# Optimization experiments

Hardware: AMD Instinct MI355X
Metric: run time of the kernel (lower is better)

Reference implementation:

```python
import jax, jax.numpy as jnp
import numpy as np

NUM_HEADS = 12


def _rel_pos_table(q_size, k_size, rel_pos):
    # rel_pos: (2*q_size-1, head_dim); q_size == k_size here so no interpolation.
    q_coords = jnp.arange(q_size)[:, None] * max(k_size / q_size, 1.0)
    k_coords = jnp.arange(k_size)[None, :] * max(q_size / k_size, 1.0)
    rel = (q_coords - k_coords + (k_size - 1) * max(q_size / k_size, 1.0)).astype(jnp.int32)
    return rel_pos[rel]  # (q_size, k_size, head_dim)


def setup_inputs() -> dict:
    key = jax.random.key(0)
    ks = jax.random.split(key, 7)
    B, H, W, D = 1, 64, 64, 768
    hd = D // NUM_HEADS
    x = jax.random.normal(ks[0], (B, H, W, D), dtype=jnp.float32)
    w_qkv = jax.random.normal(ks[1], (3 * D, D), dtype=jnp.float32) * (1.0 / np.sqrt(D))
    b_qkv = jnp.zeros((3 * D,), dtype=jnp.float32)
    w_proj = jax.random.normal(ks[2], (D, D), dtype=jnp.float32) * (1.0 / np.sqrt(D))
    b_proj = jnp.zeros((D,), dtype=jnp.float32)
    rel_pos_h = jax.random.normal(ks[3], (2 * H - 1, hd), dtype=jnp.float32) * 0.02
    rel_pos_w = jax.random.normal(ks[4], (2 * W - 1, hd), dtype=jnp.float32) * 0.02
    return {"x": x, "w_qkv": w_qkv, "b_qkv": b_qkv, "w_proj": w_proj,
            "b_proj": b_proj, "rel_pos_h": rel_pos_h, "rel_pos_w": rel_pos_w}


def reference(x, w_qkv, b_qkv, w_proj, b_proj, rel_pos_h, rel_pos_w):
    b, h, w, d = x.shape
    nh = NUM_HEADS
    hd = d // nh
    scale = hd ** -0.5
    # combined qkv projection: (b,h,w,3d) -> (3, b*nh, h*w, hd)
    qkv = x @ w_qkv.T + b_qkv
    qkv = qkv.reshape(b, h * w, 3, nh, hd).transpose(2, 0, 3, 1, 4)
    qkv = qkv.reshape(3, b * nh, h * w, hd)
    q, k, v = qkv[0], qkv[1], qkv[2]
    attn = (q * scale) @ k.swapaxes(-2, -1)  # (b*nh, hw, hw)
    # decomposed 2D relative position bias
    rh = _rel_pos_table(h, h, rel_pos_h)  # (h, h, hd)
    rw = _rel_pos_table(w, w, rel_pos_w)  # (w, w, hd)
    r_q = q.reshape(b * nh, h, w, hd)
    rel_h = jnp.einsum('bhwc,hkc->bhwk', r_q, rh)
    rel_w = jnp.einsum('bhwc,wkc->bhwk', r_q, rw)
    attn = (attn.reshape(b * nh, h, w, h, w)
            + rel_h[:, :, :, :, None]
            + rel_w[:, :, :, None, :]).reshape(b * nh, h * w, h * w)
    attn = jax.nn.softmax(attn, axis=-1)
    out = attn @ v  # (b*nh, hw, hd)
    out = out.reshape(b, nh, h, w, hd).transpose(0, 2, 3, 1, 4).reshape(b, h, w, d)
    return out @ w_proj.T + b_proj
```

## Files before the change

### kernel.cpp

```cpp
#include <hip/hip_runtime.h>
#include <hip/hip_bf16.h>
#include <stdint.h>


typedef unsigned short u16;
typedef unsigned int   u32;
typedef __attribute__((ext_vector_type(8))) short s8v;
typedef __attribute__((ext_vector_type(4))) float f4v;
typedef __attribute__((ext_vector_type(4))) unsigned short us4;
typedef __attribute__((ext_vector_type(8))) unsigned short us8;
typedef __attribute__((ext_vector_type(2))) unsigned int u32x2;

#define DEVI static __device__ __forceinline__

constexpr int   NTOK   = 4096;
constexpr int   DM     = 768;
constexpr float LOG2E_F = 1.4426950408889634f;
constexpr float KSCALE  = 0.18033688011112042f;

#if __has_builtin(__builtin_amdgcn_exp2f)
#define EXP2(x) __builtin_amdgcn_exp2f(x)
#else
#define EXP2(x) exp2f(x)
#endif

DEVI u16 f2bf(float x){
  u32 u = __builtin_bit_cast(u32, x);
  u32 r = (u + 0x7FFFu + ((u >> 16) & 1u)) >> 16;
  return (u16)r;
}
DEVI float bf2f(u16 h){
  u32 u = ((u32)h) << 16;
  return __builtin_bit_cast(float, u);
}
DEVI u32 cvtpk(float lo, float hi){
  u32 r;
  asm("v_cvt_pk_bf16_f32 %0, %1, %2" : "=v"(r) : "v"(lo), "v"(hi));
  return r;
}

typedef const __attribute__((address_space(1))) u32* gp1;
typedef __attribute__((address_space(3))) u32* lp3;
DEVI void gload_lds16(const void* g, void* l){
  __builtin_amdgcn_global_load_lds((gp1)g, (lp3)l, 16, 0, 0);
}

DEVI f4v MFMA16(s8v a, s8v b, f4v c){
  return __builtin_amdgcn_mfma_f32_16x16x32_bf16(a, b, c, 0, 0, 0);
}

__global__ void k_split(const float* __restrict__ in, u16* __restrict__ hi,
                        u16* __restrict__ lo, int n4){
  int i = blockIdx.x * blockDim.x + threadIdx.x;
  int stride = gridDim.x * blockDim.x;
  for (; i < n4; i += stride){
    f4v v = ((const f4v*)in)[i];
    us4 h, l;
#pragma unroll
    for (int j = 0; j < 4; ++j){
      u16 hb = f2bf(v[j]);
      h[j] = hb;
      l[j] = f2bf(v[j] - bf2f(hb));
    }
    ((us4*)hi)[i] = h;
    ((us4*)lo)[i] = l;
  }
}

template<int EPI>
__global__ __launch_bounds__(256)
void k_gemm(const u16* __restrict__ Ah, const u16* __restrict__ Al,
            const u16* __restrict__ Bh, const u16* __restrict__ Bl,
            const float* __restrict__ bias, int K,
            u16* __restrict__ Qh, u16* __restrict__ Ql,
            u16* __restrict__ Kh, u16* __restrict__ Kl,
            float* __restrict__ Vf, float* __restrict__ Cout)
{
  __shared__ __align__(16) unsigned char sm[32768];
  const int t = threadIdx.x;
  const int lane = t & 63, wid = t >> 6;
  const int l15 = lane & 15, g = lane >> 4;
  const int wr = wid >> 1, wc = wid & 1;
  const int m0 = blockIdx.y * 128, n0 = blockIdx.x * 128;

  const char* aGh[2]; const char* aGl[2]; const char* bGh[2]; const char* bGl[2];
#pragma unroll
  for (int ch = 0; ch < 2; ++ch){
    int p = ch * 4096 + t * 16;
    int pair = p >> 7, w = p & 127;
    int u = w ^ ((pair & 7) << 4);
    int row = 2 * pair + (u >> 6);
    int cb  = u & 63;
    aGh[ch] = (const char*)Ah + (size_t)(m0 + row) * K * 2 + cb;
    aGl[ch] = (const char*)Al + (size_t)(m0 + row) * K * 2 + cb;
    bGh[ch] = (const char*)Bh + (size_t)(n0 + row) * K * 2 + cb;
    bGl[ch] = (const char*)Bl + (size_t)(n0 + row) * K * 2 + cb;
  }
  const int axor = ((l15 & 1) * 64 + g * 16) ^ (((l15 >> 1) & 7) << 4);
  const int abase = (wr * 32 + (l15 >> 1)) * 128 + axor;
  const int bbase = 16384 + (wc * 32 + (l15 >> 1)) * 128 + axor;

  f4v acc[4][4] = {};
  const int KSTEPS = K >> 5;
  for (int kt = 0; kt < KSTEPS; ++kt){
    __syncthreads();
#pragma unroll
    for (int ch = 0; ch < 2; ++ch){
      gload_lds16(aGh[ch], sm + 0     + ch*4096 + wid*1024);
      gload_lds16(aGl[ch], sm + 8192  + ch*4096 + wid*1024);
      gload_lds16(bGh[ch], sm + 16384 + ch*4096 + wid*1024);
      gload_lds16(bGl[ch], sm + 24576 + ch*4096 + wid*1024);
      aGh[ch] += 64; aGl[ch] += 64; bGh[ch] += 64; bGl[ch] += 64;
    }
    __syncthreads();
    s8v af[4][2];
#pragma unroll
    for (int mi = 0; mi < 4; ++mi){
      af[mi][0] = *(const s8v*)(sm + abase + mi*1024);
      af[mi][1] = *(const s8v*)(sm + abase + mi*1024 + 8192);
    }
#pragma unroll
    for (int ni = 0; ni < 4; ++ni){
      s8v bh = *(const s8v*)(sm + bbase + ni*1024);
      s8v bl = *(const s8v*)(sm + bbase + ni*1024 + 8192);
#pragma unroll
      for (int mi = 0; mi < 4; ++mi){
        acc[mi][ni] = MFMA16(af[mi][0], bh, acc[mi][ni]);
        acc[mi][ni] = MFMA16(af[mi][0], bl, acc[mi][ni]);
        acc[mi][ni] = MFMA16(af[mi][1], bh, acc[mi][ni]);
      }
    }
  }

  if (EPI == 2){
#pragma unroll
    for (int ni = 0; ni < 4; ++ni){
      int col = n0 + wc*64 + ni*16 + l15;
      float bq = bias[col];
#pragma unroll
      for (int mi = 0; mi < 4; ++mi){
        int rw0 = m0 + wr*64 + mi*16 + g*4;
#pragma unroll
        for (int r = 0; r < 4; ++r)
          Cout[(size_t)(rw0 + r) * DM + col] = acc[mi][ni][r] + bq;
      }
    }
  } else {
#pragma unroll
    for (int ni = 0; ni < 4; ++ni){
      int colb = n0 + wc*64 + ni*16;
      float bq = bias[colb + l15];
      int which = colb / DM;
      int rem   = colb % DM;
      int head  = rem >> 6;
      int c     = (rem & 63) + l15;
#pragma unroll
      for (int mi = 0; mi < 4; ++mi){
        int n = m0 + wr*64 + mi*16 + g*4;
#pragma unroll
        for (int r = 0; r < 4; ++r){
          float v = acc[mi][ni][r] + bq;
          size_t idx = ((size_t)head * NTOK + (n + r)) * 64 + c;
          if (which == 0){
            u16 hb = f2bf(v);
            Qh[idx] = hb; Ql[idx] = f2bf(v - bf2f(hb));
          } else if (which == 1){
            float v2 = v * KSCALE;
            u16 hb = f2bf(v2);
            Kh[idx] = hb; Kl[idx] = f2bf(v2 - bf2f(hb));
          } else {
            Vf[idx] = v;
          }
        }
      }
    }
  }
}

__global__ void k_vtrans(const float* __restrict__ Vf, u16* __restrict__ Vth){
  __shared__ float tile[64][65];
  int h = blockIdx.y, nt = blockIdx.x;
  int t = threadIdx.x;
  {
    int r = t >> 2, c0 = (t & 3) * 16;
    const float* src = Vf + ((size_t)h * NTOK + nt*64 + r) * 64 + c0;
#pragma unroll
    for (int j = 0; j < 4; ++j){
      f4v v = *(const f4v*)(src + j*4);
      tile[r][c0+j*4+0] = v[0]; tile[r][c0+j*4+1] = v[1];
      tile[r][c0+j*4+2] = v[2]; tile[r][c0+j*4+3] = v[3];
    }
  }
  __syncthreads();
  {
    int c = t >> 2, b = (t & 3) * 16;
    us8 o0, o1;
#pragma unroll
    for (int i = 0; i < 16; ++i){
      u16 bv = f2bf(tile[b + i][c]);
      if (i < 8) o0[i] = bv; else o1[i-8] = bv;
    }
    u16* dst = Vth + ((size_t)h * 64 + c) * NTOK + nt*64 + b;
    *(us8*)(dst)     = o0;
    *(us8*)(dst + 8) = o1;
  }
}

__global__ void k_relh(const u16* __restrict__ Qh, const u16* __restrict__ Ql,
                       const float* __restrict__ rp, float* __restrict__ R){
  __shared__ float qs[64][68];
  __shared__ float rs[64][68];
  int h = blockIdx.y, qh = blockIdx.x;
  int t = threadIdx.x;
  {
    int r = t >> 2, c0 = (t & 3) * 16;
    size_t qb = ((size_t)h * NTOK + qh*64 + r) * 64 + c0;
#pragma unroll
    for (int j = 0; j < 2; ++j){
      us8 vh = *(const us8*)(Qh + qb + j*8);
      us8 vl = *(const us8*)(Ql + qb + j*8);
#pragma unroll
      for (int e = 0; e < 8; ++e)
        qs[r][c0 + j*8 + e] = bf2f(vh[e]) + bf2f(vl[e]);
    }
    const float* pr = rp + (size_t)(qh - r + 63) * 64 + c0;
#pragma unroll
    for (int j = 0; j < 4; ++j){
      f4v v = *(const f4v*)(pr + j*4);
      rs[r][c0+j*4+0]=v[0]; rs[r][c0+j*4+1]=v[1];
      rs[r][c0+j*4+2]=v[2]; rs[r][c0+j*4+3]=v[3];
    }
  }
  __syncthreads();
  int qw = t >> 2, k0 = t & 3;
  float acc[16] = {};
  for (int c = 0; c < 64; c += 4){
    f4v qv = *(const f4v*)(&qs[qw][c]);
#pragma unroll
    for (int i = 0; i < 16; ++i){
      f4v rv = *(const f4v*)(&rs[k0 + 4*i][c]);
      acc[i] += qv[0]*rv[0] + qv[1]*rv[1] + qv[2]*rv[2] + qv[3]*rv[3];
    }
  }
  float* o = R + ((size_t)h * NTOK + qh*64 + qw) * 64;
#pragma unroll
  for (int i = 0; i < 16; ++i) o[k0 + 4*i] = acc[i] * LOG2E_F;
}

__global__ void k_relw(const u16* __restrict__ Qh, const u16* __restrict__ Ql,
                       const float* __restrict__ rp, float* __restrict__ R){
  __shared__ float qs[64][68];
  __shared__ float rs[64][68];
  int h = blockIdx.y, qw = blockIdx.x;
  int t = threadIdx.x;
  {
    int r = t >> 2, c0 = (t & 3) * 16;
    size_t qb = ((size_t)h * NTOK + r*64 + qw) * 64 + c0;
#pragma unroll
    for (int j = 0; j < 2; ++j){
      us8 vh = *(const us8*)(Qh + qb + j*8);
      us8 vl = *(const us8*)(Ql + qb + j*8);
#pragma unroll
      for (int e = 0; e < 8; ++e)
        qs[r][c0 + j*8 + e] = bf2f(vh[e]) + bf2f(vl[e]);
    }
    const float* pr = rp + (size_t)(qw - r + 63) * 64 + c0;
#pragma unroll
    for (int j = 0; j < 4; ++j){
      f4v v = *(const f4v*)(pr + j*4);
      rs[r][c0+j*4+0]=v[0]; rs[r][c0+j*4+1]=v[1];
      rs[r][c0+j*4+2]=v[2]; rs[r][c0+j*4+3]=v[3];
    }
  }
  __syncthreads();
  int qh = t >> 2, k0 = t & 3;
  float acc[16] = {};
  for (int c = 0; c < 64; c += 4){
    f4v qv = *(const f4v*)(&qs[qh][c]);
#pragma unroll
    for (int i = 0; i < 16; ++i){
      f4v rv = *(const f4v*)(&rs[k0 + 4*i][c]);
      acc[i] += qv[0]*rv[0] + qv[1]*rv[1] + qv[2]*rv[2] + qv[3]*rv[3];
    }
  }
  float* o = R + ((size_t)h * NTOK + qh*64 + qw) * 64;
#pragma unroll
  for (int i = 0; i < 16; ++i) o[k0 + 4*i] = acc[i] * LOG2E_F;
}

__global__ __launch_bounds__(256)
void k_attn(const u16* __restrict__ Qh, const u16* __restrict__ Ql,
            const u16* __restrict__ Kh, const u16* __restrict__ Kl,
            const u16* __restrict__ Vth,
            const float* __restrict__ Rh, const float* __restrict__ Rw,
            u16* __restrict__ Oh, u16* __restrict__ Ol)
{
  __shared__ __align__(16) unsigned char sm[33792];
  const int t = threadIdx.x;
  const int lane = t & 63, wid = t >> 6;
  const int l15 = lane & 15, g = lane >> 4;
  const int h = blockIdx.y;
  const int qrow0 = blockIdx.x * 64 + wid * 16;

  const char* kGh[2]; const char* kGl[2]; const char* vG[2];
#pragma unroll
  for (int ch = 0; ch < 2; ++ch){
    int p = ch * 4096 + t * 16;
    int row = p >> 7;
    int cb  = (p & 127) ^ ((row & 7) << 4);
    kGh[ch] = (const char*)Kh + ((size_t)h * NTOK + row) * 128 + cb;
    kGl[ch] = (const char*)Kl + ((size_t)h * NTOK + row) * 128 + cb;
    vG[ch]  = (const char*)Vth + ((size_t)h * 64 + row) * (NTOK*2) + cb;
  }

  const size_t qoff = ((size_t)h * NTOK + qrow0 + l15) * 64 + g * 8;
  s8v qh0 = *(const s8v*)(Qh + qoff);
  s8v qh1 = *(const s8v*)(Qh + qoff + 32);
  s8v ql0 = *(const s8v*)(Ql + qoff);
  s8v ql1 = *(const s8v*)(Ql + qoff + 32);

  const int xr  = (l15 & 7) << 4;
  const int kb0 = l15 * 128 + ((g * 16)      ^ xr);
  const int kb1 = l15 * 128 + ((g * 16 + 64) ^ xr);
  const int vb0 = 16384 + kb0;
  const int vb1 = 16384 + kb1;
  const int pbase = 24576 + wid * 2304 + l15 * 144;

  const float* rwp = Rw + ((size_t)h * NTOK + qrow0 + l15) * 64 + 4*g;
  f4v rwv[4];
#pragma unroll
  for (int tt = 0; tt < 4; ++tt) rwv[tt] = *(const f4v*)(rwp + 16*tt);
  const float* rhp = Rh + ((size_t)h * NTOK + qrow0 + l15) * 64;

  f4v o[4] = {};
  float m2 = -1.0e30f, ls = 0.f;

  for (int it = 0; it < 64; ++it){
    __syncthreads();
#pragma unroll
    for (int ch = 0; ch < 2; ++ch){
      gload_lds16(kGh[ch], sm + 0     + ch*4096 + wid*1024);
      gload_lds16(kGl[ch], sm + 8192  + ch*4096 + wid*1024);
      gload_lds16(vG[ch],  sm + 16384 + ch*4096 + wid*1024);
      kGh[ch] += 8192; kGl[ch] += 8192; vG[ch] += 128;
    }
    __syncthreads();

    const float rhv = rhp[it];

    f4v s[4];
#pragma unroll
    for (int tt = 0; tt < 4; ++tt){
      s8v kh_0 = *(const s8v*)(sm + kb0 + tt*2048);
      s8v kh_1 = *(const s8v*)(sm + kb1 + tt*2048);
      s8v kl_0 = *(const s8v*)(sm + kb0 + tt*2048 + 8192);
      s8v kl_1 = *(const s8v*)(sm + kb1 + tt*2048 + 8192);
      f4v a = {};
      a = MFMA16(kh_0, qh0, a);
      a = MFMA16(kh_1, qh1, a);
      a = MFMA16(kl_0, qh0, a);
      a = MFMA16(kl_1, qh1, a);
      a = MFMA16(kh_0, ql0, a);
      a = MFMA16(kh_1, ql1, a);
      s[tt] = a;
    }
    float pm = -1.0e30f;
#pragma unroll
    for (int tt = 0; tt < 4; ++tt){
#pragma unroll
      for (int r = 0; r < 4; ++r){
        s[tt][r] += rhv + rwv[tt][r];
        pm = fmaxf(pm, s[tt][r]);
      }
    }
    pm = fmaxf(pm, __shfl_xor(pm, 16, 64));
    pm = fmaxf(pm, __shfl_xor(pm, 32, 64));
    const float mn = fmaxf(m2, pm);
    const float fr = EXP2(m2 - mn);
    m2 = mn;
    float ps = 0.f;
#pragma unroll
    for (int tt = 0; tt < 4; ++tt){
#pragma unroll
      for (int r = 0; r < 4; ++r){
        float p = EXP2(s[tt][r] - m2);
        s[tt][r] = p;
        ps += p;
      }
    }
    ps += __shfl_xor(ps, 16, 64);
    ps += __shfl_xor(ps, 32, 64);
    ls = ls * fr + ps;

#pragma unroll
    for (int tt = 0; tt < 4; ++tt){
      u32x2 w2;
      w2[0] = cvtpk(s[tt][0], s[tt][1]);
      w2[1] = cvtpk(s[tt][2], s[tt][3]);
      *(u32x2*)(sm + pbase + 8*g + 32*tt) = w2;
    }
#pragma unroll
    for (int dt = 0; dt < 4; ++dt){
#pragma unroll
      for (int r = 0; r < 4; ++r) o[dt][r] *= fr;
    }
    s8v pa0 = *(const s8v*)(sm + pbase + 16*g);
    s8v pa1 = *(const s8v*)(sm + pbase + 16*g + 64);
#pragma unroll
    for (int dt = 0; dt < 4; ++dt){
      s8v v0 = *(const s8v*)(sm + vb0 + dt*2048);
      s8v v1 = *(const s8v*)(sm + vb1 + dt*2048);
      o[dt] = MFMA16(v0, pa0, o[dt]);
      o[dt] = MFMA16(v1, pa1, o[dt]);
    }
  }

  const float inv = 1.0f / ls;
  const size_t obase = (size_t)(qrow0 + l15) * DM + h*64 + 4*g;
#pragma unroll
  for (int dt = 0; dt < 4; ++dt){
    us4 hv, lv;
#pragma unroll
    for (int r = 0; r < 4; ++r){
      float v = o[dt][r] * inv;
      u16 hb = f2bf(v);
      hv[r] = hb;
      lv[r] = f2bf(v - bf2f(hb));
    }
    *(us4*)(Oh + obase + 16*dt) = hv;
    *(us4*)(Ol + obase + 16*dt) = lv;
  }
}

extern "C" void kernel_launch(void* const* d_in, const int* in_sizes, int n_in,
                              void* d_out, int out_size, void* d_ws, size_t ws_size,
                              hipStream_t stream){
  (void)in_sizes; (void)n_in; (void)out_size; (void)ws_size;
  const float* x      = (const float*)d_in[0];
  const float* w_qkv  = (const float*)d_in[1];
  const float* b_qkv  = (const float*)d_in[2];
  const float* w_proj = (const float*)d_in[3];
  const float* b_proj = (const float*)d_in[4];
  const float* rph    = (const float*)d_in[5];
  const float* rpw    = (const float*)d_in[6];
  float* out = (float*)d_out;

  char* w = (char*)d_ws;
  size_t off = 0;
  auto nxt = [&](size_t b) -> char* {
    char* p = w + off; off += (b + 255) & ~(size_t)255; return p;
  };
  u16*   Xh  = (u16*)  nxt((size_t)NTOK*DM*2);
  u16*   Xl  = (u16*)  nxt((size_t)NTOK*DM*2);
  u16*   Wqh = (u16*)  nxt((size_t)3*DM*DM*2);
  u16*   Wql = (u16*)  nxt((size_t)3*DM*DM*2);
  u16*   Wph = (u16*)  nxt((size_t)DM*DM*2);
  u16*   Wpl = (u16*)  nxt((size_t)DM*DM*2);
  u16*   Qh  = (u16*)  nxt((size_t)NTOK*DM*2);
  u16*   Ql  = (u16*)  nxt((size_t)NTOK*DM*2);
  u16*   Kh  = (u16*)  nxt((size_t)NTOK*DM*2);
  u16*   Kl  = (u16*)  nxt((size_t)NTOK*DM*2);
  float* Vf  = (float*)nxt((size_t)NTOK*DM*4);
  u16*   Vth = (u16*)  nxt((size_t)NTOK*DM*2);
  float* Rh  = (float*)nxt((size_t)12*NTOK*64*4);
  float* Rw  = (float*)nxt((size_t)12*NTOK*64*4);
  u16*   Oh  = Xh;
  u16*   Ol  = Xl;

  k_split<<<dim3(3072), dim3(256), 0, stream>>>(x,      Xh,  Xl,  NTOK*DM/4);
  k_split<<<dim3(1728), dim3(256), 0, stream>>>(w_qkv,  Wqh, Wql, 3*DM*DM/4);
  k_split<<<dim3(576),  dim3(256), 0, stream>>>(w_proj, Wph, Wpl, DM*DM/4);

  k_gemm<1><<<dim3(18, 32), dim3(256), 0, stream>>>(
      Xh, Xl, Wqh, Wql, b_qkv, DM, Qh, Ql, Kh, Kl, Vf, nullptr);

  k_vtrans<<<dim3(64, 12), dim3(256), 0, stream>>>(Vf, Vth);
  k_relh  <<<dim3(64, 12), dim3(256), 0, stream>>>(Qh, Ql, rph, Rh);
  k_relw  <<<dim3(64, 12), dim3(256), 0, stream>>>(Qh, Ql, rpw, Rw);

  k_attn<<<dim3(64, 12), dim3(256), 0, stream>>>(Qh, Ql, Kh, Kl, Vth, Rh, Rw, Oh, Ol);

  k_gemm<2><<<dim3(6, 32), dim3(256), 0, stream>>>(
      Oh, Ol, Wph, Wpl, b_proj, DM,
      nullptr, nullptr, nullptr, nullptr, nullptr, out);
}
```

Baseline: 377.8 us.

## Double-buffer LDS tiles in GEMM and attention with prefetch and priority hints

```diff
diff --git a/kernel.cpp b/kernel.cpp
--- a/kernel.cpp
+++ b/kernel.cpp
@@ -47,6 +47,14 @@
 
 DEVI f4v MFMA16(s8v a, s8v b, f4v c){
   return __builtin_amdgcn_mfma_f32_16x16x32_bf16(a, b, c, 0, 0, 0);
+}
+
+DEVI void hard_barrier(){
+  __builtin_amdgcn_sched_barrier(0);
+  asm volatile("" ::: "memory");
+  __builtin_amdgcn_s_barrier();
+  asm volatile("" ::: "memory");
+  __builtin_amdgcn_sched_barrier(0);
 }
 
 __global__ void k_split(const float* __restrict__ in, u16* __restrict__ hi,
@@ -76,7 +84,7 @@
             u16* __restrict__ Kh, u16* __restrict__ Kl,
             float* __restrict__ Vf, float* __restrict__ Cout)
 {
-  __shared__ __align__(16) unsigned char sm[32768];
+  __shared__ __align__(16) unsigned char sm[65536];
   const int t = threadIdx.x;
   const int lane = t & 63, wid = t >> 6;
   const int l15 = lane & 15, g = lane >> 4;
@@ -100,29 +108,46 @@
   const int abase = (wr * 32 + (l15 >> 1)) * 128 + axor;
   const int bbase = 16384 + (wc * 32 + (l15 >> 1)) * 128 + axor;
 
+#pragma unroll
+  for (int ch = 0; ch < 2; ++ch){
+    gload_lds16(aGh[ch], sm + 0     + ch*4096 + wid*1024);
+    gload_lds16(aGl[ch], sm + 8192  + ch*4096 + wid*1024);
+    gload_lds16(bGh[ch], sm + 16384 + ch*4096 + wid*1024);
+    gload_lds16(bGl[ch], sm + 24576 + ch*4096 + wid*1024);
+    aGh[ch] += 64; aGl[ch] += 64; bGh[ch] += 64; bGl[ch] += 64;
+  }
+
   f4v acc[4][4] = {};
   const int KSTEPS = K >> 5;
   for (int kt = 0; kt < KSTEPS; ++kt){
-    __syncthreads();
-#pragma unroll
-    for (int ch = 0; ch < 2; ++ch){
-      gload_lds16(aGh[ch], sm + 0     + ch*4096 + wid*1024);
-      gload_lds16(aGl[ch], sm + 8192  + ch*4096 + wid*1024);
-      gload_lds16(bGh[ch], sm + 16384 + ch*4096 + wid*1024);
-      gload_lds16(bGl[ch], sm + 24576 + ch*4096 + wid*1024);
-      aGh[ch] += 64; aGl[ch] += 64; bGh[ch] += 64; bGl[ch] += 64;
-    }
-    __syncthreads();
+    const int bb = (kt & 1) * 32768;
+    if (kt + 1 < KSTEPS){
+      const int nb = ((kt + 1) & 1) * 32768;
+#pragma unroll
+      for (int ch = 0; ch < 2; ++ch){
+        gload_lds16(aGh[ch], sm + nb + 0     + ch*4096 + wid*1024);
+        gload_lds16(aGl[ch], sm + nb + 8192  + ch*4096 + wid*1024);
+        gload_lds16(bGh[ch], sm + nb + 16384 + ch*4096 + wid*1024);
+        gload_lds16(bGl[ch], sm + nb + 24576 + ch*4096 + wid*1024);
+        aGh[ch] += 64; aGl[ch] += 64; bGh[ch] += 64; bGl[ch] += 64;
+      }
+      asm volatile("s_waitcnt vmcnt(8)" ::: "memory");
+    } else {
+      asm volatile("s_waitcnt vmcnt(0)" ::: "memory");
+    }
+    hard_barrier();
+
     s8v af[4][2];
 #pragma unroll
     for (int mi = 0; mi < 4; ++mi){
-      af[mi][0] = *(const s8v*)(sm + abase + mi*1024);
-      af[mi][1] = *(const s8v*)(sm + abase + mi*1024 + 8192);
-    }
+      af[mi][0] = *(const s8v*)(sm + bb + abase + mi*1024);
+      af[mi][1] = *(const s8v*)(sm + bb + abase + mi*1024 + 8192);
+    }
+    __builtin_amdgcn_s_setprio(1);
 #pragma unroll
     for (int ni = 0; ni < 4; ++ni){
-      s8v bh = *(const s8v*)(sm + bbase + ni*1024);
-      s8v bl = *(const s8v*)(sm + bbase + ni*1024 + 8192);
+      s8v bh = *(const s8v*)(sm + bb + bbase + ni*1024);
+      s8v bl = *(const s8v*)(sm + bb + bbase + ni*1024 + 8192);
 #pragma unroll
       for (int mi = 0; mi < 4; ++mi){
         acc[mi][ni] = MFMA16(af[mi][0], bh, acc[mi][ni]);
@@ -130,6 +155,8 @@
         acc[mi][ni] = MFMA16(af[mi][1], bh, acc[mi][ni]);
       }
     }
+    __builtin_amdgcn_s_setprio(0);
+    hard_barrier();
   }
 
   if (EPI == 2){
@@ -295,7 +322,8 @@
             const float* __restrict__ Rh, const float* __restrict__ Rw,
             u16* __restrict__ Oh, u16* __restrict__ Ol)
 {
-  __shared__ __align__(16) unsigned char sm[33792];
+  constexpr int BUF1 = 24576, POFF = 49152, RHOFF = 58368;
+  __shared__ __align__(16) unsigned char sm[75776];
   const int t = threadIdx.x;
   const int lane = t & 63, wid = t >> 6;
   const int l15 = lane & 15, g = lane >> 4;
@@ -313,6 +341,17 @@
     vG[ch]  = (const char*)Vth + ((size_t)h * 64 + row) * (NTOK*2) + cb;
   }
 
+  {
+    const char* rhg = (const char*)(Rh + ((size_t)h * NTOK + blockIdx.x * 64) * 64);
+#pragma unroll
+    for (int s2 = 0; s2 < 4; ++s2){
+      int off = s2*4096 + t*16;
+      f4v v = *(const f4v*)(rhg + off);
+      *(f4v*)(sm + RHOFF + (off >> 8) * 272 + (off & 255)) = v;
+    }
+  }
+  asm volatile("s_waitcnt lgkmcnt(0)" ::: "memory");
+
   const size_t qoff = ((size_t)h * NTOK + qrow0 + l15) * 64 + g * 8;
   s8v qh0 = *(const s8v*)(Qh + qoff);
   s8v qh1 = *(const s8v*)(Qh + qoff + 32);
@@ -324,37 +363,52 @@
   const int kb1 = l15 * 128 + ((g * 16 + 64) ^ xr);
   const int vb0 = 16384 + kb0;
   const int vb1 = 16384 + kb1;
-  const int pbase = 24576 + wid * 2304 + l15 * 144;
+  const int pbase = POFF + wid * 2304 + l15 * 144;
+  const int rhrd  = RHOFF + (wid * 16 + l15) * 272;
 
   const float* rwp = Rw + ((size_t)h * NTOK + qrow0 + l15) * 64 + 4*g;
   f4v rwv[4];
 #pragma unroll
   for (int tt = 0; tt < 4; ++tt) rwv[tt] = *(const f4v*)(rwp + 16*tt);
-  const float* rhp = Rh + ((size_t)h * NTOK + qrow0 + l15) * 64;
+
+#pragma unroll
+  for (int ch = 0; ch < 2; ++ch){
+    gload_lds16(kGh[ch], sm + 0     + ch*4096 + wid*1024);
+    gload_lds16(kGl[ch], sm + 8192  + ch*4096 + wid*1024);
+    gload_lds16(vG[ch],  sm + 16384 + ch*4096 + wid*1024);
+    kGh[ch] += 8192; kGl[ch] += 8192; vG[ch] += 128;
+  }
 
   f4v o[4] = {};
   float m2 = -1.0e30f, ls = 0.f;
 
   for (int it = 0; it < 64; ++it){
-    __syncthreads();
-#pragma unroll
-    for (int ch = 0; ch < 2; ++ch){
-      gload_lds16(kGh[ch], sm + 0     + ch*4096 + wid*1024);
-      gload_lds16(kGl[ch], sm + 8192  + ch*4096 + wid*1024);
-      gload_lds16(vG[ch],  sm + 16384 + ch*4096 + wid*1024);
-      kGh[ch] += 8192; kGl[ch] += 8192; vG[ch] += 128;
-    }
-    __syncthreads();
-
-    const float rhv = rhp[it];
+    const int bb = (it & 1) * BUF1;
+    if (it < 63){
+      const int nb = ((it + 1) & 1) * BUF1;
+#pragma unroll
+      for (int ch = 0; ch < 2; ++ch){
+        gload_lds16(kGh[ch], sm + nb + 0     + ch*4096 + wid*1024);
+        gload_lds16(kGl[ch], sm + nb + 8192  + ch*4096 + wid*1024);
+        gload_lds16(vG[ch],  sm + nb + 16384 + ch*4096 + wid*1024);
+        kGh[ch] += 8192; kGl[ch] += 8192; vG[ch] += 128;
+      }
+      asm volatile("s_waitcnt vmcnt(6)" ::: "memory");
+    } else {
+      asm volatile("s_waitcnt vmcnt(0)" ::: "memory");
+    }
+    hard_barrier();
+
+    const float rhv = *(const float*)(sm + rhrd + it * 4);
 
     f4v s[4];
+    __builtin_amdgcn_s_setprio(1);
 #pragma unroll
     for (int tt = 0; tt < 4; ++tt){
-      s8v kh_0 = *(const s8v*)(sm + kb0 + tt*2048);
-      s8v kh_1 = *(const s8v*)(sm + kb1 + tt*2048);
-      s8v kl_0 = *(const s8v*)(sm + kb0 + tt*2048 + 8192);
-      s8v kl_1 = *(const s8v*)(sm + kb1 + tt*2048 + 8192);
+      s8v kh_0 = *(const s8v*)(sm + bb + kb0 + tt*2048);
+      s8v kh_1 = *(const s8v*)(sm + bb + kb1 + tt*2048);
+      s8v kl_0 = *(const s8v*)(sm + bb + kb0 + tt*2048 + 8192);
+      s8v kl_1 = *(const s8v*)(sm + bb + kb1 + tt*2048 + 8192);
       f4v a = {};
       a = MFMA16(kh_0, qh0, a);
       a = MFMA16(kh_1, qh1, a);
@@ -364,6 +418,8 @@
       a = MFMA16(kh_1, ql1, a);
       s[tt] = a;
     }
+    __builtin_amdgcn_s_setprio(0);
+
     float pm = -1.0e30f;
 #pragma unroll
     for (int tt = 0; tt < 4; ++tt){
@@ -406,13 +462,17 @@
     }
     s8v pa0 = *(const s8v*)(sm + pbase + 16*g);
     s8v pa1 = *(const s8v*)(sm + pbase + 16*g + 64);
+    __builtin_amdgcn_s_setprio(1);
 #pragma unroll
     for (int dt = 0; dt < 4; ++dt){
-      s8v v0 = *(const s8v*)(sm + vb0 + dt*2048);
-      s8v v1 = *(const s8v*)(sm + vb1 + dt*2048);
+      s8v v0 = *(const s8v*)(sm + bb + vb0 + dt*2048);
+      s8v v1 = *(const s8v*)(sm + bb + vb1 + dt*2048);
       o[dt] = MFMA16(v0, pa0, o[dt]);
       o[dt] = MFMA16(v1, pa1, o[dt]);
     }
+    __builtin_amdgcn_s_setprio(0);
+
+    hard_barrier();
   }
 
   const float inv = 1.0f / ls;
```

New measurement: 373.5 us. Within noise of the previous version (-1.1%).
